# Kernel tuning notes

Hardware: AMD Instinct MI355X
Metric: run time of the kernel (lower is better)

## Reference

```python
import jax, jax.numpy as jnp
import numpy as np

D = 512  # input_size
H = 512  # hidden_size
N = 64   # batch
T = 512  # timesteps


def setup_inputs() -> dict:
    key = jax.random.key(0)
    k1, k2, k3, k4 = jax.random.split(key, 4)
    x = jax.random.normal(k1, (N, T, D), dtype=jnp.float32)
    h0 = jax.random.normal(k2, (N, H), dtype=jnp.float32)
    Wx = jax.random.normal(k3, (D, H), dtype=jnp.float32) / np.sqrt(D)
    Wh = jax.random.normal(k4, (H, H), dtype=jnp.float32) / np.sqrt(H)
    b = jnp.zeros((H,), dtype=jnp.float32)
    return {"x": x, "h0": h0, "Wx": Wx, "Wh": Wh, "b": b}


def reference(x, h0, Wx, Wh, b):
    # Precompute input projections for all timesteps in one big GEMM:
    # same math as per-step x_t @ Wx inside the loop.
    xWx = jnp.einsum('ntd,dh->nth', x, Wx) + b  # (N, T, H)

    def step(prev_h, xwx_t):
        next_h = jnp.tanh(prev_h @ Wh + xwx_t)  # (N, H)
        return next_h, next_h

    # scan over time: xWx transposed to (T, N, H)
    _, hs = jax.lax.scan(step, h0, jnp.swapaxes(xWx, 0, 1))
    return jnp.swapaxes(hs, 0, 1)  # (N, T, H)
```

## Files before the change

kernel.cpp:

```cpp
#include <hip/hip_runtime.h>
#include <hip/hip_bf16.h>

#define NB 64
#define TT 512
#define HH 512
#define DD 512

typedef __attribute__((ext_vector_type(8))) __bf16 bf16x8;
typedef __attribute__((ext_vector_type(4))) float f32x4;

__device__ __forceinline__ unsigned short f2bf_rn(float f) {
    union { float f; unsigned u; } v; v.f = f;
    unsigned r = v.u + 0x7FFFu + ((v.u >> 16) & 1u);
    return (unsigned short)(r >> 16);
}
__device__ __forceinline__ float bf2f(unsigned short s) {
    union { unsigned u; float f; } v; v.u = ((unsigned)s) << 16;
    return v.f;
}

__global__ __launch_bounds__(256) void wt_kernel(const float* __restrict__ Wx,
                                                 unsigned short* __restrict__ Wt) {
    const int bk = blockIdx.x >> 3, bn = blockIdx.x & 7;
    const int k0 = bk * 64, n0 = bn * 64;
    __shared__ float tile[64][65];
    const int t = threadIdx.x;
    const int kr = t >> 2, seg = t & 3;
    const float4* src = (const float4*)&Wx[(k0 + kr) * HH + n0 + seg * 16];
    float4 a = src[0], b = src[1], c = src[2], d = src[3];
    float vv[16];
    *(float4*)&vv[0] = a; *(float4*)&vv[4] = b; *(float4*)&vv[8] = c; *(float4*)&vv[12] = d;
#pragma unroll
    for (int q = 0; q < 16; ++q) tile[kr][seg * 16 + q] = vv[q];
    __syncthreads();
    const int nr = t >> 2;
    unsigned hu[8], lu[8];
#pragma unroll
    for (int i = 0; i < 8; ++i) {
        float f0 = tile[seg * 16 + 2 * i + 0][nr];
        float f1 = tile[seg * 16 + 2 * i + 1][nr];
        unsigned short h0 = f2bf_rn(f0); unsigned short l0 = f2bf_rn(f0 - bf2f(h0));
        unsigned short h1 = f2bf_rn(f1); unsigned short l1 = f2bf_rn(f1 - bf2f(h1));
        hu[i] = (unsigned)h0 | ((unsigned)h1 << 16);
        lu[i] = (unsigned)l0 | ((unsigned)l1 << 16);
    }
    unsigned short* dh = &Wt[(n0 + nr) * 1024 + k0 + seg * 16];
    unsigned short* dl = dh + 512;
    ((uint4*)dh)[0] = make_uint4(hu[0], hu[1], hu[2], hu[3]);
    ((uint4*)dh)[1] = make_uint4(hu[4], hu[5], hu[6], hu[7]);
    ((uint4*)dl)[0] = make_uint4(lu[0], lu[1], lu[2], lu[3]);
    ((uint4*)dl)[1] = make_uint4(lu[4], lu[5], lu[6], lu[7]);
}

#define LDA 72
__global__ __launch_bounds__(256) void proj_kernel(const float* __restrict__ x,
                                                   const unsigned short* __restrict__ Wt,
                                                   const float* __restrict__ bias,
                                                   float* __restrict__ out) {
    __shared__ __align__(16) unsigned short a_hi[64 * LDA];
    __shared__ __align__(16) unsigned short a_lo[64 * LDA];
    __shared__ __align__(16) unsigned short b_hi[64 * LDA];
    __shared__ __align__(16) unsigned short b_lo[64 * LDA];

    const int bx = blockIdx.x;
    const int i0 = (bx >> 3) * 64;
    const int n0 = (bx & 7) * 64;
    const int t = threadIdx.x;
    const int row = t >> 2, seg = t & 3;
    const int lane = t & 63, wid = t >> 6;
    const int wm = (wid >> 1) * 32, wn = (wid & 1) * 32;
    const int fr = lane & 15;

    f32x4 acc00 = {0.f, 0.f, 0.f, 0.f}, acc01 = acc00, acc10 = acc00, acc11 = acc00;

    for (int kc = 0; kc < 8; ++kc) {
        __syncthreads();
        {
            const float4* src = (const float4*)&x[(i0 + row) * DD + kc * 64 + seg * 16];
            float4 a = src[0], b = src[1], c = src[2], d = src[3];
            float vv[16];
            *(float4*)&vv[0] = a; *(float4*)&vv[4] = b; *(float4*)&vv[8] = c; *(float4*)&vv[12] = d;
            unsigned hu[8], lu[8];
#pragma unroll
            for (int i = 0; i < 8; ++i) {
                unsigned short h0 = f2bf_rn(vv[2 * i]); unsigned short l0 = f2bf_rn(vv[2 * i] - bf2f(h0));
                unsigned short h1 = f2bf_rn(vv[2 * i + 1]); unsigned short l1 = f2bf_rn(vv[2 * i + 1] - bf2f(h1));
                hu[i] = (unsigned)h0 | ((unsigned)h1 << 16);
                lu[i] = (unsigned)l0 | ((unsigned)l1 << 16);
            }
            uint4* dh = (uint4*)&a_hi[row * LDA + seg * 16];
            uint4* dl = (uint4*)&a_lo[row * LDA + seg * 16];
            dh[0] = make_uint4(hu[0], hu[1], hu[2], hu[3]);
            dh[1] = make_uint4(hu[4], hu[5], hu[6], hu[7]);
            dl[0] = make_uint4(lu[0], lu[1], lu[2], lu[3]);
            dl[1] = make_uint4(lu[4], lu[5], lu[6], lu[7]);
        }
        {
            const uint4* sh = (const uint4*)&Wt[(n0 + row) * 1024 + kc * 64 + seg * 16];
            const uint4* sl = (const uint4*)&Wt[(n0 + row) * 1024 + 512 + kc * 64 + seg * 16];
            uint4 h0v = sh[0], h1v = sh[1], l0v = sl[0], l1v = sl[1];
            uint4* dh = (uint4*)&b_hi[row * LDA + seg * 16];
            uint4* dl = (uint4*)&b_lo[row * LDA + seg * 16];
            dh[0] = h0v; dh[1] = h1v; dl[0] = l0v; dl[1] = l1v;
        }
        __syncthreads();
#pragma unroll
        for (int s = 0; s < 2; ++s) {
            const int ko = s * 32 + (lane >> 4) * 8;
            bf16x8 ah0 = *(const bf16x8*)&a_hi[(wm + fr) * LDA + ko];
            bf16x8 ah1 = *(const bf16x8*)&a_hi[(wm + 16 + fr) * LDA + ko];
            bf16x8 al0 = *(const bf16x8*)&a_lo[(wm + fr) * LDA + ko];
            bf16x8 al1 = *(const bf16x8*)&a_lo[(wm + 16 + fr) * LDA + ko];
            bf16x8 bh0 = *(const bf16x8*)&b_hi[(wn + fr) * LDA + ko];
            bf16x8 bh1 = *(const bf16x8*)&b_hi[(wn + 16 + fr) * LDA + ko];
            bf16x8 bl0 = *(const bf16x8*)&b_lo[(wn + fr) * LDA + ko];
            bf16x8 bl1 = *(const bf16x8*)&b_lo[(wn + 16 + fr) * LDA + ko];
            acc00 = __builtin_amdgcn_mfma_f32_16x16x32_bf16(ah0, bh0, acc00, 0, 0, 0);
            acc00 = __builtin_amdgcn_mfma_f32_16x16x32_bf16(ah0, bl0, acc00, 0, 0, 0);
            acc00 = __builtin_amdgcn_mfma_f32_16x16x32_bf16(al0, bh0, acc00, 0, 0, 0);
            acc01 = __builtin_amdgcn_mfma_f32_16x16x32_bf16(ah0, bh1, acc01, 0, 0, 0);
            acc01 = __builtin_amdgcn_mfma_f32_16x16x32_bf16(ah0, bl1, acc01, 0, 0, 0);
            acc01 = __builtin_amdgcn_mfma_f32_16x16x32_bf16(al0, bh1, acc01, 0, 0, 0);
            acc10 = __builtin_amdgcn_mfma_f32_16x16x32_bf16(ah1, bh0, acc10, 0, 0, 0);
            acc10 = __builtin_amdgcn_mfma_f32_16x16x32_bf16(ah1, bl0, acc10, 0, 0, 0);
            acc10 = __builtin_amdgcn_mfma_f32_16x16x32_bf16(al1, bh0, acc10, 0, 0, 0);
            acc11 = __builtin_amdgcn_mfma_f32_16x16x32_bf16(ah1, bh1, acc11, 0, 0, 0);
            acc11 = __builtin_amdgcn_mfma_f32_16x16x32_bf16(ah1, bl1, acc11, 0, 0, 0);
            acc11 = __builtin_amdgcn_mfma_f32_16x16x32_bf16(al1, bh1, acc11, 0, 0, 0);
        }
    }
    const float bc0 = bias[n0 + wn + fr];
    const float bc1 = bias[n0 + wn + 16 + fr];
#pragma unroll
    for (int r = 0; r < 4; ++r) {
        int rw0 = i0 + wm + (lane >> 4) * 4 + r;
        int rw1 = rw0 + 16;
        out[rw0 * HH + n0 + wn + fr]      = acc00[r] + bc0;
        out[rw0 * HH + n0 + wn + 16 + fr] = acc01[r] + bc1;
        out[rw1 * HH + n0 + wn + fr]      = acc10[r] + bc0;
        out[rw1 * HH + n0 + wn + 16 + fr] = acc11[r] + bc1;
    }
}

__global__ __launch_bounds__(512, 2) void rec_kernel(const float* __restrict__ h0,
                                                     const float* __restrict__ Wh,
                                                     float* __restrict__ out,
                                                     unsigned long long* __restrict__ hbuf2) {
    const int b = blockIdx.x;
    const int g = b & 63;
    const int s = b >> 6;
    const int c0 = s * 128;
    const int tid = threadIdx.x;
    const int jl = tid & 127;
    const int kg = tid >> 7;
    const int kb = kg * 128;
    const int j = c0 + jl;

    float w[128];
#pragma unroll
    for (int r = 0; r < 128; ++r) w[r] = Wh[(kb + r) * HH + j];

    __shared__ float hs[HH];
    __shared__ float red[3][128];

    float xw = (kg == 0) ? out[(g * TT + 0) * HH + j] : 0.f;

#pragma unroll 1
    for (int t = 0; t < TT; ++t) {
        if (t == 0) {
            hs[tid] = h0[g * HH + tid];
        } else if (tid < c0 || tid >= c0 + 128) {
            const unsigned long long* slot =
                &hbuf2[(((unsigned)(t + 1)) & 1u) * (NB * HH) + g * HH + tid];
            unsigned long long v;
            do {
                v = __hip_atomic_load(slot, __ATOMIC_RELAXED, __HIP_MEMORY_SCOPE_AGENT);
            } while ((unsigned)(v >> 32) != (unsigned)t);
            hs[tid] = __uint_as_float((unsigned)v);
        }
        __syncthreads();

        float p0 = 0.f, p1 = 0.f, p2 = 0.f, p3 = 0.f;
        const float4* h4 = (const float4*)&hs[kb];
#pragma unroll
        for (int r4 = 0; r4 < 32; ++r4) {
            float4 hv = h4[r4];
            p0 = fmaf(w[4 * r4 + 0], hv.x, p0);
            p1 = fmaf(w[4 * r4 + 1], hv.y, p1);
            p2 = fmaf(w[4 * r4 + 2], hv.z, p2);
            p3 = fmaf(w[4 * r4 + 3], hv.w, p3);
        }
        float p = (p0 + p1) + (p2 + p3);

        if (kg) red[kg - 1][jl] = p;
        __syncthreads();
        if (kg == 0) {
            float v = p + red[0][jl] + red[1][jl] + red[2][jl] + xw;
            float hn = 1.f - 2.f / (__expf(2.f * v) + 1.f);
            unsigned long long pv =
                (((unsigned long long)(unsigned)(t + 1)) << 32) |
                (unsigned long long)__float_as_uint(hn);
            __hip_atomic_store(&hbuf2[((unsigned)t & 1u) * (NB * HH) + g * HH + j], pv,
                               __ATOMIC_RELAXED, __HIP_MEMORY_SCOPE_AGENT);
            hs[j] = hn;
            out[(g * TT + t) * HH + j] = hn;
            if (t + 1 < TT) xw = out[(g * TT + t + 1) * HH + j];
        }
    }
}

extern "C" void kernel_launch(void* const* d_in, const int* in_sizes, int n_in,
                              void* d_out, int out_size, void* d_ws, size_t ws_size,
                              hipStream_t stream) {
    (void)in_sizes; (void)n_in; (void)out_size; (void)ws_size;
    const float* x  = (const float*)d_in[0];
    const float* h0 = (const float*)d_in[1];
    const float* Wx = (const float*)d_in[2];
    const float* Wh = (const float*)d_in[3];
    const float* bv = (const float*)d_in[4];
    float* out = (float*)d_out;

    unsigned long long* hbuf2 = (unsigned long long*)d_ws;
    unsigned short* Wt = (unsigned short*)((char*)d_ws + 2 * NB * HH * sizeof(unsigned long long));

    hipMemsetAsync(hbuf2, 0, 2 * NB * HH * sizeof(unsigned long long), stream);

    wt_kernel<<<64, 256, 0, stream>>>(Wx, Wt);

    proj_kernel<<<(32768 / 64) * (HH / 64), 256, 0, stream>>>(x, Wt, bv, out);

    rec_kernel<<<NB * 4, 512, 0, stream>>>(h0, Wh, out, hbuf2);
}
```

Baseline: 881.5 us.

## Interleave two batch rows per recurrent block to overlap cross-block waits

Each recurrent block now handles two batch rows (A and B) for its 128-column slice, alternating between them. While it computes one row's step it has already issued the atomic poll for the other row's peer data, hiding the inter-block exchange latency behind useful work. The grid shrinks from 256 blocks to 128. The price is twice the serial compute per block each timestep and fewer blocks spread across the CUs.

```diff
diff --git a/kernel.cpp b/kernel.cpp
--- a/kernel.cpp
+++ b/kernel.cpp
@@ -147,64 +147,111 @@
                                                      float* __restrict__ out,
                                                      unsigned long long* __restrict__ hbuf2) {
     const int b = blockIdx.x;
-    const int g = b & 63;
-    const int s = b >> 6;
+    const int p = b >> 2;
+    const int s = b & 3;
+    const int gA = 2 * p, gB = 2 * p + 1;
     const int c0 = s * 128;
     const int tid = threadIdx.x;
     const int jl = tid & 127;
     const int kg = tid >> 7;
     const int kb = kg * 128;
     const int j = c0 + jl;
+    const bool rem = (tid < c0) || (tid >= c0 + 128);
 
     float w[128];
 #pragma unroll
     for (int r = 0; r < 128; ++r) w[r] = Wh[(kb + r) * HH + j];
 
-    __shared__ float hs[HH];
+    __shared__ float hsA[HH], hsB[HH];
     __shared__ float red[3][128];
 
-    float xw = (kg == 0) ? out[(g * TT + 0) * HH + j] : 0.f;
+    float xwA = 0.f, xwB = 0.f;
+    if (kg == 0) {
+        xwA = out[(gA * TT + 0) * HH + j];
+        xwB = out[(gB * TT + 0) * HH + j];
+    }
+    hsA[tid] = h0[gA * HH + tid];
+    hsB[tid] = h0[gB * HH + tid];
+    __syncthreads();
 
 #pragma unroll 1
     for (int t = 0; t < TT; ++t) {
-        if (t == 0) {
-            hs[tid] = h0[g * HH + tid];
-        } else if (tid < c0 || tid >= c0 + 128) {
-            const unsigned long long* slot =
-                &hbuf2[(((unsigned)(t + 1)) & 1u) * (NB * HH) + g * HH + tid];
-            unsigned long long v;
-            do {
-                v = __hip_atomic_load(slot, __ATOMIC_RELAXED, __HIP_MEMORY_SCOPE_AGENT);
-            } while ((unsigned)(v >> 32) != (unsigned)t);
-            hs[tid] = __uint_as_float((unsigned)v);
-        }
-        __syncthreads();
-
-        float p0 = 0.f, p1 = 0.f, p2 = 0.f, p3 = 0.f;
-        const float4* h4 = (const float4*)&hs[kb];
-#pragma unroll
-        for (int r4 = 0; r4 < 32; ++r4) {
-            float4 hv = h4[r4];
-            p0 = fmaf(w[4 * r4 + 0], hv.x, p0);
-            p1 = fmaf(w[4 * r4 + 1], hv.y, p1);
-            p2 = fmaf(w[4 * r4 + 2], hv.z, p2);
-            p3 = fmaf(w[4 * r4 + 3], hv.w, p3);
-        }
-        float p = (p0 + p1) + (p2 + p3);
-
-        if (kg) red[kg - 1][jl] = p;
-        __syncthreads();
-        if (kg == 0) {
-            float v = p + red[0][jl] + red[1][jl] + red[2][jl] + xw;
-            float hn = 1.f - 2.f / (__expf(2.f * v) + 1.f);
-            unsigned long long pv =
-                (((unsigned long long)(unsigned)(t + 1)) << 32) |
-                (unsigned long long)__float_as_uint(hn);
-            __hip_atomic_store(&hbuf2[((unsigned)t & 1u) * (NB * HH) + g * HH + j], pv,
-                               __ATOMIC_RELAXED, __HIP_MEMORY_SCOPE_AGENT);
-            hs[j] = hn;
-            out[(g * TT + t) * HH + j] = hn;
-            if (t + 1 < TT) xw = out[(g * TT + t + 1) * HH + j];
+        const unsigned long long* slotB =
+            &hbuf2[(((unsigned)(t + 1)) & 1u) * (NB * HH) + gB * HH + tid];
+        unsigned long long vB = 0;
+        if (t > 0 && rem) vB = __hip_atomic_load(slotB, __ATOMIC_RELAXED, __HIP_MEMORY_SCOPE_AGENT);
+
+        {
+            float p0 = 0.f, p1 = 0.f, p2 = 0.f, p3 = 0.f;
+            const float4* h4 = (const float4*)&hsA[kb];
+#pragma unroll
+            for (int r4 = 0; r4 < 32; ++r4) {
+                float4 hv = h4[r4];
+                p0 = fmaf(w[4 * r4 + 0], hv.x, p0);
+                p1 = fmaf(w[4 * r4 + 1], hv.y, p1);
+                p2 = fmaf(w[4 * r4 + 2], hv.z, p2);
+                p3 = fmaf(w[4 * r4 + 3], hv.w, p3);
+            }
+            float pA = (p0 + p1) + (p2 + p3);
+            if (kg) red[kg - 1][jl] = pA;
+            __syncthreads();
+            if (kg == 0) {
+                float v = pA + red[0][jl] + red[1][jl] + red[2][jl] + xwA;
+                float hn = 1.f - 2.f / (__expf(2.f * v) + 1.f);
+                unsigned long long pv =
+                    (((unsigned long long)(unsigned)(t + 1)) << 32) |
+                    (unsigned long long)__float_as_uint(hn);
+                __hip_atomic_store(&hbuf2[((unsigned)t & 1u) * (NB * HH) + gA * HH + j], pv,
+                                   __ATOMIC_RELAXED, __HIP_MEMORY_SCOPE_AGENT);
+                hsA[j] = hn;
+                out[(gA * TT + t) * HH + j] = hn;
+                if (t + 1 < TT) xwA = out[(gA * TT + t + 1) * HH + j];
+            }
+            if (t > 0 && rem) {
+                while ((unsigned)(vB >> 32) != (unsigned)t)
+                    vB = __hip_atomic_load(slotB, __ATOMIC_RELAXED, __HIP_MEMORY_SCOPE_AGENT);
+                hsB[tid] = __uint_as_float((unsigned)vB);
+            }
+            __syncthreads();
+        }
+
+        const unsigned long long* slotA =
+            &hbuf2[(((unsigned)t) & 1u) * (NB * HH) + gA * HH + tid];
+        unsigned long long vA = 0;
+        if (rem) vA = __hip_atomic_load(slotA, __ATOMIC_RELAXED, __HIP_MEMORY_SCOPE_AGENT);
+
+        {
+            float p0 = 0.f, p1 = 0.f, p2 = 0.f, p3 = 0.f;
+            const float4* h4 = (const float4*)&hsB[kb];
+#pragma unroll
+            for (int r4 = 0; r4 < 32; ++r4) {
+                float4 hv = h4[r4];
+                p0 = fmaf(w[4 * r4 + 0], hv.x, p0);
+                p1 = fmaf(w[4 * r4 + 1], hv.y, p1);
+                p2 = fmaf(w[4 * r4 + 2], hv.z, p2);
+                p3 = fmaf(w[4 * r4 + 3], hv.w, p3);
+            }
+            float pB = (p0 + p1) + (p2 + p3);
+            if (kg) red[kg - 1][jl] = pB;
+            __syncthreads();
+            if (kg == 0) {
+                float v = pB + red[0][jl] + red[1][jl] + red[2][jl] + xwB;
+                float hn = 1.f - 2.f / (__expf(2.f * v) + 1.f);
+                unsigned long long pv =
+                    (((unsigned long long)(unsigned)(t + 1)) << 32) |
+                    (unsigned long long)__float_as_uint(hn);
+                __hip_atomic_store(&hbuf2[((unsigned)t & 1u) * (NB * HH) + gB * HH + j], pv,
+                                   __ATOMIC_RELAXED, __HIP_MEMORY_SCOPE_AGENT);
+                hsB[j] = hn;
+                out[(gB * TT + t) * HH + j] = hn;
+                if (t + 1 < TT) xwB = out[(gB * TT + t + 1) * HH + j];
+            }
+            if (rem) {
+                while ((unsigned)(vA >> 32) != (unsigned)(t + 1))
+                    vA = __hip_atomic_load(slotA, __ATOMIC_RELAXED, __HIP_MEMORY_SCOPE_AGENT);
+                hsA[tid] = __uint_as_float((unsigned)vA);
+            }
+            __syncthreads();
         }
     }
 }
@@ -229,5 +276,5 @@
 
     proj_kernel<<<(32768 / 64) * (HH / 64), 256, 0, stream>>>(x, Wt, bv, out);
 
-    rec_kernel<<<NB * 4, 512, 0, stream>>>(h0, Wh, out, hbuf2);
-}
+    rec_kernel<<<NB * 2, 512, 0, stream>>>(h0, Wh, out, hbuf2);
+}
```

Result: slower. 1.231 ms (+39.6%).

## Split recurrent matvec by k-slice and exchange partial sums instead of hidden state

Applied to the files above, without the earlier changes.

Each block now holds a 128-row slice of Wh and computes partial dot products for all 512 output columns, publishing tagged partials to the block that owns each column slice. The owner threads poll the three remote partials, add their own plus the input projection, apply tanh, and keep their own h slice locally in double-buffered LDS. This removes the full-h gather and the in-block LDS reduction from each step, at the cost of three times more cross-block traffic per step.

```diff
diff --git a/kernel.cpp b/kernel.cpp
--- a/kernel.cpp
+++ b/kernel.cpp
@@ -145,43 +145,33 @@
 __global__ __launch_bounds__(512, 2) void rec_kernel(const float* __restrict__ h0,
                                                      const float* __restrict__ Wh,
                                                      float* __restrict__ out,
-                                                     unsigned long long* __restrict__ hbuf2) {
+                                                     unsigned long long* __restrict__ pbuf) {
     const int b = blockIdx.x;
     const int g = b & 63;
     const int s = b >> 6;
-    const int c0 = s * 128;
-    const int tid = threadIdx.x;
-    const int jl = tid & 127;
-    const int kg = tid >> 7;
-    const int kb = kg * 128;
-    const int j = c0 + jl;
+    const int j = threadIdx.x;
+    const int sj = j >> 7;
+    const bool owner = (sj == s);
+    const int jl = j & 127;
+    const int idx = s - (s > sj ? 1 : 0);
 
     float w[128];
 #pragma unroll
-    for (int r = 0; r < 128; ++r) w[r] = Wh[(kb + r) * HH + j];
-
-    __shared__ float hs[HH];
-    __shared__ float red[3][128];
-
-    float xw = (kg == 0) ? out[(g * TT + 0) * HH + j] : 0.f;
+    for (int r = 0; r < 128; ++r) w[r] = Wh[(s * 128 + r) * HH + j];
+
+    __shared__ float hsl[2][128];
+    if (j < 128) hsl[0][j] = h0[g * HH + s * 128 + j];
+
+    float xw = owner ? out[(g * TT + 0) * HH + j] : 0.f;
+    __syncthreads();
 
 #pragma unroll 1
     for (int t = 0; t < TT; ++t) {
-        if (t == 0) {
-            hs[tid] = h0[g * HH + tid];
-        } else if (tid < c0 || tid >= c0 + 128) {
-            const unsigned long long* slot =
-                &hbuf2[(((unsigned)(t + 1)) & 1u) * (NB * HH) + g * HH + tid];
-            unsigned long long v;
-            do {
-                v = __hip_atomic_load(slot, __ATOMIC_RELAXED, __HIP_MEMORY_SCOPE_AGENT);
-            } while ((unsigned)(v >> 32) != (unsigned)t);
-            hs[tid] = __uint_as_float((unsigned)v);
-        }
-        __syncthreads();
+        const int slot = t & 1;
+        const unsigned tg = (unsigned)(t + 1);
 
         float p0 = 0.f, p1 = 0.f, p2 = 0.f, p3 = 0.f;
-        const float4* h4 = (const float4*)&hs[kb];
+        const float4* h4 = (const float4*)&hsl[t & 1][0];
 #pragma unroll
         for (int r4 = 0; r4 < 32; ++r4) {
             float4 hv = h4[r4];
@@ -190,22 +180,33 @@
             p2 = fmaf(w[4 * r4 + 2], hv.z, p2);
             p3 = fmaf(w[4 * r4 + 3], hv.w, p3);
         }
-        float p = (p0 + p1) + (p2 + p3);
-
-        if (kg) red[kg - 1][jl] = p;
+        float part = (p0 + p1) + (p2 + p3);
+
+        if (!owner) {
+            unsigned long long pv = ((unsigned long long)tg << 32) |
+                                    (unsigned long long)__float_as_uint(part);
+            __hip_atomic_store(&pbuf[(((unsigned)slot * NB + g) * 3 + idx) * HH + j], pv,
+                               __ATOMIC_RELAXED, __HIP_MEMORY_SCOPE_AGENT);
+        } else {
+            float xwn = (t + 1 < TT) ? out[(g * TT + t + 1) * HH + j] : 0.f;
+            const unsigned long long* a0 = &pbuf[(((unsigned)slot * NB + g) * 3 + 0) * HH + j];
+            const unsigned long long* a1 = a0 + HH;
+            const unsigned long long* a2 = a1 + HH;
+            unsigned long long v0, v1, v2;
+            do {
+                v0 = __hip_atomic_load(a0, __ATOMIC_RELAXED, __HIP_MEMORY_SCOPE_AGENT);
+                v1 = __hip_atomic_load(a1, __ATOMIC_RELAXED, __HIP_MEMORY_SCOPE_AGENT);
+                v2 = __hip_atomic_load(a2, __ATOMIC_RELAXED, __HIP_MEMORY_SCOPE_AGENT);
+            } while ((unsigned)(v0 >> 32) != tg || (unsigned)(v1 >> 32) != tg ||
+                     (unsigned)(v2 >> 32) != tg);
+            float v = part + __uint_as_float((unsigned)v0) + __uint_as_float((unsigned)v1) +
+                      __uint_as_float((unsigned)v2) + xw;
+            float hn = 1.f - 2.f / (__expf(2.f * v) + 1.f);
+            out[(g * TT + t) * HH + j] = hn;
+            hsl[(t + 1) & 1][jl] = hn;
+            xw = xwn;
+        }
         __syncthreads();
-        if (kg == 0) {
-            float v = p + red[0][jl] + red[1][jl] + red[2][jl] + xw;
-            float hn = 1.f - 2.f / (__expf(2.f * v) + 1.f);
-            unsigned long long pv =
-                (((unsigned long long)(unsigned)(t + 1)) << 32) |
-                (unsigned long long)__float_as_uint(hn);
-            __hip_atomic_store(&hbuf2[((unsigned)t & 1u) * (NB * HH) + g * HH + j], pv,
-                               __ATOMIC_RELAXED, __HIP_MEMORY_SCOPE_AGENT);
-            hs[j] = hn;
-            out[(g * TT + t) * HH + j] = hn;
-            if (t + 1 < TT) xw = out[(g * TT + t + 1) * HH + j];
-        }
     }
 }
 
@@ -220,14 +221,15 @@
     const float* bv = (const float*)d_in[4];
     float* out = (float*)d_out;
 
-    unsigned long long* hbuf2 = (unsigned long long*)d_ws;
-    unsigned short* Wt = (unsigned short*)((char*)d_ws + 2 * NB * HH * sizeof(unsigned long long));
-
-    hipMemsetAsync(hbuf2, 0, 2 * NB * HH * sizeof(unsigned long long), stream);
+    const size_t PBUF_BYTES = 2ull * NB * 3 * HH * sizeof(unsigned long long);
+    unsigned long long* pbuf = (unsigned long long*)d_ws;
+    unsigned short* Wt = (unsigned short*)((char*)d_ws + PBUF_BYTES);
+
+    hipMemsetAsync(pbuf, 0, PBUF_BYTES, stream);
 
     wt_kernel<<<64, 256, 0, stream>>>(Wx, Wt);
 
     proj_kernel<<<(32768 / 64) * (HH / 64), 256, 0, stream>>>(x, Wt, bv, out);
 
-    rec_kernel<<<NB * 4, 512, 0, stream>>>(h0, Wh, out, hbuf2);
-}
+    rec_kernel<<<NB * 4, 512, 0, stream>>>(h0, Wh, out, pbuf);
+}
```

Measured after the change: 898.8 us. Within noise of the previous version (+2.0%).
